# Kernel tuning notes

Hardware: AMD Instinct MI355X
Metric: run time of the kernel (lower is better)

The kernel has to match this reference:

```python
import jax, jax.numpy as jnp
import numpy as np

D_MODEL = 768
STATE_N = 16
BATCH = 8
SEQ = 2048


def setup_inputs() -> dict:
    key = jax.random.key(0)
    ks = jax.random.split(key, 12)
    d, n = D_MODEL, STATE_N
    s = 0.02
    inp = {
        "x": jax.random.normal(ks[0], (BATCH, SEQ, d), dtype=jnp.float32),
        # A_log init as in module: log(arange(1..N)) repeated over d_model
        "A_log": jnp.log(jnp.tile(jnp.arange(1, n + 1, dtype=jnp.float32)[None, :], (d, 1))),
        "D_param": jnp.ones((d,), dtype=jnp.float32),
        "B_proj_w": jax.random.normal(ks[1], (n, d), dtype=jnp.float32) * s,
        "C_proj_w": jax.random.normal(ks[2], (n, d), dtype=jnp.float32) * s,
        "delta_w": jax.random.normal(ks[3], (d, d), dtype=jnp.float32) * s,
        "delta_b": jax.random.normal(ks[4], (d,), dtype=jnp.float32) * s,
        "in_w": jax.random.normal(ks[5], (2 * d, d), dtype=jnp.float32) * s,
        "in_b": jax.random.normal(ks[6], (2 * d,), dtype=jnp.float32) * s,
        "out_w": jax.random.normal(ks[7], (d, d), dtype=jnp.float32) * s,
        "out_b": jax.random.normal(ks[8], (d,), dtype=jnp.float32) * s,
        "conv_w": jax.random.normal(ks[9], (d, 1, 3), dtype=jnp.float32) * s,  # depthwise [D,1,K]
        "conv_b": jax.random.normal(ks[10], (d,), dtype=jnp.float32) * s,
    }
    return inp


def _forward(x, A_log, D_param, B_proj_w, C_proj_w, delta_w, delta_b,
             in_w, in_b, out_w, out_b, conv_w, conv_b):
    A = -jnp.exp(A_log)  # [D, N]
    xz = jnp.einsum("bld,ed->ble", x, in_w) + in_b  # [B, L, 2D]
    x_in, z = jnp.split(xz, 2, axis=-1)
    # depthwise conv1d, padding=1, groups=D (cross-correlation, same as torch)
    x_c = jax.lax.conv_general_dilated(
        jnp.transpose(x_in, (0, 2, 1)), conv_w,
        window_strides=(1,), padding=((1, 1),),
        feature_group_count=x.shape[-1],
        dimension_numbers=("NCH", "OIH", "NCH"))
    x_conv = jnp.transpose(x_c, (0, 2, 1)) + conv_b  # [B, L, D]
    x_conv = jax.nn.silu(x_conv)
    delta = jax.nn.softplus(jnp.einsum("bld,ed->ble", x_conv, delta_w) + delta_b)  # [B,L,D]
    B_sel = jnp.einsum("bld,nd->bln", x_conv, B_proj_w)  # [B, L, N]
    C_sel = jnp.einsum("bld,nd->bln", x_conv, C_proj_w)  # [B, L, N]

    Bsz, L, D = x.shape
    N = A.shape[1]

    def step(h, t_in):
        dt, b_t, c_t, x_t = t_in  # [B,D], [B,N], [B,N], [B,D]
        A_bar = jnp.exp(dt[:, :, None] * A[None, :, :])           # [B,D,N]
        h = A_bar * h + (dt[:, :, None] * b_t[:, None, :]) * x_t[:, :, None]
        y_t = jnp.sum(h * c_t[:, None, :], axis=-1)               # [B,D]
        return h, y_t

    xs = (jnp.transpose(delta, (1, 0, 2)), jnp.transpose(B_sel, (1, 0, 2)),
          jnp.transpose(C_sel, (1, 0, 2)), jnp.transpose(x_conv, (1, 0, 2)))
    h0 = jnp.zeros((Bsz, D, N), dtype=x.dtype)
    _, ys = jax.lax.scan(step, h0, xs)
    y = jnp.transpose(ys, (1, 0, 2))  # [B, L, D]

    y = y + x_conv * D_param[None, None, :]
    y = y * jax.nn.silu(z)
    return jnp.einsum("bld,ed->ble", y, out_w) + out_b


def reference(x, A_log, D_param, B_proj_w, C_proj_w, delta_w, delta_b,
              in_w, in_b, out_w, out_b, conv_w, conv_b):
    return _forward(x, A_log, D_param, B_proj_w, C_proj_w, delta_w, delta_b,
                    in_w, in_b, out_w, out_b, conv_w, conv_b)
```

## Files before the change

### kernel.cpp

```cpp
#include <hip/hip_runtime.h>
#include <hip/hip_bf16.h>

#define D_MODEL 768
#define SEQL    2048
#define BATCH   8
#define NSTATE  16
#define NCHUNK  32
#define TCHUNK  64

typedef __attribute__((ext_vector_type(8))) short short8;
typedef __attribute__((ext_vector_type(4))) float f32x4;

typedef const __attribute__((address_space(1))) unsigned int gas1_t;
typedef __attribute__((address_space(3))) unsigned int las3_t;

__device__ __forceinline__ void gload_lds16(const void* g, void* l) {
  __builtin_amdgcn_global_load_lds((gas1_t*)g, (las3_t*)l, 16, 0, 0);
}

__global__ __launch_bounds__(256) void prep_all(
    const float* __restrict__ x, const float* __restrict__ in_w,
    const float* __restrict__ delta_w, const float* __restrict__ Bp,
    const float* __restrict__ Cp, const float* __restrict__ out_w,
    const float* __restrict__ A_log,
    __hip_bfloat16* __restrict__ xb, __hip_bfloat16* __restrict__ w_in,
    __hip_bfloat16* __restrict__ w_dbc, __hip_bfloat16* __restrict__ w_out,
    float* __restrict__ A2) {
  int i = blockIdx.x * 256 + threadIdx.x;
  if (i < 3145728) {
    int j = i * 4;
    float4 v = *(const float4*)(x + j);
    xb[j + 0] = __float2bfloat16(v.x);
    xb[j + 1] = __float2bfloat16(v.y);
    xb[j + 2] = __float2bfloat16(v.z);
    xb[j + 3] = __float2bfloat16(v.w);
    return;
  }
  i -= 3145728;
  if (i < 1536 * 768) { w_in[i] = __float2bfloat16(in_w[i]); return; }
  i -= 1536 * 768;
  if (i < 1024 * 768) {
    int row = i / 768, col = i - row * 768;
    float v;
    if (row < 768)      v = delta_w[row * 768 + col];
    else if (row < 784) v = Bp[(row - 768) * 768 + col];
    else if (row < 800) v = Cp[(row - 784) * 768 + col];
    else                v = 0.f;
    w_dbc[i] = __float2bfloat16(v);
    return;
  }
  i -= 1024 * 768;
  if (i < 768 * 768) { w_out[i] = __float2bfloat16(out_w[i]); return; }
  i -= 768 * 768;
  A2[i] = -expf(A_log[i]) * 1.44269504088896f;
}

template <int MODE>
__global__ __launch_bounds__(512, 2) void gemm256(
    const __hip_bfloat16* __restrict__ Amat, const __hip_bfloat16* __restrict__ Bw,
    const float* __restrict__ bias, void* __restrict__ out0,
    void* __restrict__ out1, void* __restrict__ out2, const int gxn) {
  constexpr int K = 768;
  __shared__ char lds[131072];
  const int tid  = threadIdx.x;
  const int lane = tid & 63, wave = tid >> 6;
  const int wr = wave >> 2, wc = wave & 3;

  const int nwg = gridDim.x, id = blockIdx.x;
  const int swz = (id & 7) * (nwg >> 3) + (id >> 3);
  const int tm = swz / gxn, tn = swz - tm * gxn;
  const int rowA0 = tm * 256, rowB0 = tn * 256;

  const int srow0 = tid >> 3;
  const int scol  = (((tid & 7) ^ (srow0 & 7)) << 3);
  const __hip_bfloat16* gA = Amat + (size_t)(rowA0 + srow0) * K + scol;
  const __hip_bfloat16* gB = Bw   + (size_t)(rowB0 + srow0) * K + scol;
  const int ldst = tid << 4;

  const int frow = lane & 15, fq = lane >> 4;
  const int fswz = (frow & 7) << 4;
  const int pc0 = (fq << 4) ^ fswz;
  const int pc1 = (64 | (fq << 4)) ^ fswz;
  const int aro = (wr * 64 + frow) << 7;
  const int bro = (wc * 32 + frow) << 7;

  f32x4 acc[2][2][4][2];
#pragma unroll
  for (int mh = 0; mh < 2; ++mh)
#pragma unroll
    for (int nh = 0; nh < 2; ++nh)
#pragma unroll
      for (int m = 0; m < 4; ++m)
#pragma unroll
        for (int n = 0; n < 2; ++n) acc[mh][nh][m][n] = (f32x4){0.f, 0.f, 0.f, 0.f};

#define STAGE_AH(d, h, kt)                                                      \
  {                                                                             \
    const __hip_bfloat16* s0 = gA + (size_t)((h)*128) * K + (kt)*64;            \
    char* d0 = lds + ((d) << 16) + ((h) << 14) + ldst;                          \
    gload_lds16(s0, d0);                                                        \
    gload_lds16(s0 + (size_t)64 * K, d0 + 8192);                                \
  }
#define STAGE_BH(d, h, kt)                                                      \
  {                                                                             \
    const __hip_bfloat16* s0 = gB + (size_t)((h)*128) * K + (kt)*64;            \
    char* d0 = lds + ((d) << 16) + 32768 + ((h) << 14) + ldst;                  \
    gload_lds16(s0, d0);                                                        \
    gload_lds16(s0 + (size_t)64 * K, d0 + 8192);                                \
  }

  short8 a[4][2], b[2][2];
#define LOADA(d, mh)                                                            \
  {                                                                             \
    const char* base = lds + ((d) << 16) + ((mh) << 14) + aro;                  \
    _Pragma("unroll") for (int m = 0; m < 4; ++m) {                             \
      const char* p = base + ((m * 16) << 7);                                   \
      a[m][0] = *(const short8*)(p + pc0);                                      \
      a[m][1] = *(const short8*)(p + pc1);                                      \
    }                                                                           \
  }
#define LOADB(d, nh)                                                            \
  {                                                                             \
    const char* base = lds + ((d) << 16) + 32768 + ((nh) << 14) + bro;          \
    _Pragma("unroll") for (int n = 0; n < 2; ++n) {                             \
      const char* p = base + ((n * 16) << 7);                                   \
      b[n][0] = *(const short8*)(p + pc0);                                      \
      b[n][1] = *(const short8*)(p + pc1);                                      \
    }                                                                           \
  }
#define MMA(mh, nh)                                                             \
  {                                                                             \
    __builtin_amdgcn_s_setprio(1);                                              \
    _Pragma("unroll") for (int m = 0; m < 4; ++m)                               \
    _Pragma("unroll") for (int n = 0; n < 2; ++n)                               \
    _Pragma("unroll") for (int ks = 0; ks < 2; ++ks)                            \
        acc[mh][nh][m][n] = __builtin_amdgcn_mfma_f32_16x16x32_bf16(            \
            a[m][ks], b[n][ks], acc[mh][nh][m][n], 0, 0, 0);                    \
    __builtin_amdgcn_s_setprio(0);                                              \
  }
#define VMW(n) asm volatile("s_waitcnt vmcnt(" #n ")" ::: "memory")

  STAGE_AH(0, 0, 0);
  STAGE_BH(0, 0, 0);
  STAGE_BH(0, 1, 0);
  STAGE_AH(0, 1, 0);

  constexpr int NT = K / 64;
  for (int kt = 0; kt < NT - 1; ++kt) {
    const int cur = kt & 1, nxt = cur ^ 1;
    VMW(4);
    __builtin_amdgcn_s_barrier();
    LOADA(cur, 0);
    LOADB(cur, 0);
    STAGE_AH(nxt, 0, kt + 1);
    MMA(0, 0);
    VMW(4);
    __builtin_amdgcn_s_barrier();
    LOADB(cur, 1);
    STAGE_BH(nxt, 0, kt + 1);
    MMA(0, 1);
    VMW(4);
    __builtin_amdgcn_s_barrier();
    LOADA(cur, 1);
    STAGE_BH(nxt, 1, kt + 1);
    MMA(1, 1);
    __builtin_amdgcn_s_barrier();
    LOADB(cur, 0);
    STAGE_AH(nxt, 1, kt + 1);
    MMA(1, 0);
  }
  {
    const int cur = (NT - 1) & 1;
    VMW(4);
    __builtin_amdgcn_s_barrier();
    LOADA(cur, 0);
    LOADB(cur, 0);
    MMA(0, 0);
    VMW(2);
    __builtin_amdgcn_s_barrier();
    LOADB(cur, 1);
    MMA(0, 1);
    VMW(0);
    __builtin_amdgcn_s_barrier();
    LOADA(cur, 1);
    MMA(1, 1);
    __builtin_amdgcn_s_barrier();
    LOADB(cur, 0);
    MMA(1, 0);
  }

#pragma unroll
  for (int mh = 0; mh < 2; ++mh)
#pragma unroll
    for (int nh = 0; nh < 2; ++nh)
#pragma unroll
      for (int m = 0; m < 4; ++m) {
        const int grow0 = rowA0 + mh * 128 + wr * 64 + m * 16 + fq * 4;
#pragma unroll
        for (int n = 0; n < 2; ++n) {
          const int gcol = rowB0 + nh * 128 + wc * 32 + n * 16 + frow;
#pragma unroll
          for (int i = 0; i < 4; ++i) {
            const size_t grow = grow0 + i;
            float v = acc[mh][nh][m][n][i];
            if (MODE == 0) {
              v += bias[gcol];
              if (gcol < 768)
                ((__hip_bfloat16*)out0)[grow * 768 + gcol] = __float2bfloat16(v);
              else
                ((__hip_bfloat16*)out1)[grow * 768 + gcol - 768] = __float2bfloat16(v);
            } else if (MODE == 1) {
              if (gcol < 768) {
                v += bias[gcol];
                float sp = (v > 20.f) ? v : log1pf(expf(v));
                ((__hip_bfloat16*)out0)[grow * 768 + gcol] = __float2bfloat16(sp);
              } else if (gcol < 784) {
                ((float*)out1)[grow * 16 + (gcol - 768)] = v;
              } else if (gcol < 800) {
                ((float*)out2)[grow * 16 + (gcol - 784)] = v;
              }
            } else {
              ((float*)out0)[grow * 768 + gcol] = v + bias[gcol];
            }
          }
        }
      }
#undef STAGE_AH
#undef STAGE_BH
#undef LOADA
#undef LOADB
#undef MMA
#undef VMW
}

__global__ __launch_bounds__(256) void conv_silu(
    const __hip_bfloat16* __restrict__ xin, const float* __restrict__ conv_w,
    const float* __restrict__ conv_b, __hip_bfloat16* __restrict__ xc) {
  const int idx = blockIdx.x * 256 + threadIdx.x;
  const int d = idx % 768;
  const int t = (idx / 768) % SEQL;
  const float w0 = conv_w[d * 3], w1 = conv_w[d * 3 + 1], w2 = conv_w[d * 3 + 2];
  float acc = conv_b[d];
  float xm = (t > 0)        ? __bfloat162float(xin[idx - 768]) : 0.f;
  float x0 = __bfloat162float(xin[idx]);
  float xp = (t < SEQL - 1) ? __bfloat162float(xin[idx + 768]) : 0.f;
  acc += w0 * xm + w1 * x0 + w2 * xp;
  const float sig = 1.f / (1.f + __expf(-acc));
  xc[idx] = __float2bfloat16(acc * sig);
}

__global__ __launch_bounds__(256) void scan_pass1(
    const __hip_bfloat16* __restrict__ delta, const __hip_bfloat16* __restrict__ xconv,
    const float* __restrict__ Bsel, const float* __restrict__ A2,
    float* __restrict__ sumdt, float* __restrict__ Sbuf) {
  const int d = blockIdx.x * 256 + threadIdx.x;
  const int b = blockIdx.y, c = blockIdx.z;
  __shared__ float sB[TCHUNK * 16];
  ((float4*)sB)[threadIdx.x] =
      ((const float4*)(Bsel + ((size_t)b * SEQL + c * TCHUNK) * 16))[threadIdx.x];
  __syncthreads();

  float a2[16];
#pragma unroll
  for (int n = 0; n < 16; ++n) a2[n] = A2[d * 16 + n];
  float h[16] = {};
  float sdt = 0.f;
  const size_t base = ((size_t)b * SEQL + c * TCHUNK) * 768 + d;
  for (int t = 0; t < TCHUNK; ++t) {
    const float dt = __bfloat162float(delta[base + (size_t)t * 768]);
    const float x = __bfloat162float(xconv[base + (size_t)t * 768]);
    sdt += dt;
    const float dtx = dt * x;
    const float* Br = &sB[t * 16];
#pragma unroll
    for (int n = 0; n < 16; ++n) {
      const float a = exp2f(dt * a2[n]);
      h[n] = fmaf(a, h[n], dtx * Br[n]);
    }
  }
  sumdt[((size_t)b * NCHUNK + c) * 768 + d] = sdt;
#pragma unroll
  for (int n = 0; n < 16; ++n)
    Sbuf[(((size_t)b * NCHUNK + c) * 16 + n) * 768 + d] = h[n];
}

__global__ __launch_bounds__(256) void scan_carry(
    const float* __restrict__ sumdt, const float* __restrict__ Sbuf,
    const float* __restrict__ A2, float* __restrict__ Hin) {
  const int idx = blockIdx.x * 256 + threadIdx.x;
  const int d = idx % 768;
  const int n = (idx / 768) & 15;
  const int b = idx / (768 * 16);
  const float a2 = A2[d * 16 + n];
  float h = 0.f;
  for (int c = 0; c < NCHUNK; ++c) {
    const size_t hb = (((size_t)(b * NCHUNK + c)) * 16 + n) * 768 + d;
    Hin[hb] = h;
    const float sd = sumdt[(b * NCHUNK + c) * 768 + d];
    h = fmaf(exp2f(sd * a2), h, Sbuf[hb]);
  }
}

__global__ __launch_bounds__(256) void scan_pass3(
    const __hip_bfloat16* __restrict__ delta, const __hip_bfloat16* __restrict__ xconv,
    const __hip_bfloat16* __restrict__ zb, const float* __restrict__ Bsel,
    const float* __restrict__ Csel, const float* __restrict__ A2,
    const float* __restrict__ Hin, const float* __restrict__ Dp,
    __hip_bfloat16* __restrict__ yg) {
  const int d = blockIdx.x * 256 + threadIdx.x;
  const int b = blockIdx.y, c = blockIdx.z;
  __shared__ float sB[TCHUNK * 16], sC[TCHUNK * 16];
  {
    const size_t off = ((size_t)b * SEQL + c * TCHUNK) * 16;
    ((float4*)sB)[threadIdx.x] = ((const float4*)(Bsel + off))[threadIdx.x];
    ((float4*)sC)[threadIdx.x] = ((const float4*)(Csel + off))[threadIdx.x];
  }
  __syncthreads();

  float a2[16];
#pragma unroll
  for (int n = 0; n < 16; ++n) a2[n] = A2[d * 16 + n];
  float h[16];
  {
    const size_t hb = ((size_t)b * NCHUNK + c) * 16 * 768 + d;
#pragma unroll
    for (int n = 0; n < 16; ++n) h[n] = Hin[hb + (size_t)n * 768];
  }
  const float Dpd = Dp[d];
  const size_t base = ((size_t)b * SEQL + c * TCHUNK) * 768 + d;
  for (int t = 0; t < TCHUNK; ++t) {
    const float dt = __bfloat162float(delta[base + (size_t)t * 768]);
    const float x = __bfloat162float(xconv[base + (size_t)t * 768]);
    const float dtx = dt * x;
    const float* Br = &sB[t * 16];
    const float* Cr = &sC[t * 16];
    float y = 0.f;
#pragma unroll
    for (int n = 0; n < 16; ++n) {
      const float a = exp2f(dt * a2[n]);
      h[n] = fmaf(a, h[n], dtx * Br[n]);
      y = fmaf(h[n], Cr[n], y);
    }
    const float z = __bfloat162float(zb[base + (size_t)t * 768]);
    const float sig = 1.f / (1.f + __expf(-z));
    const float out = (y + x * Dpd) * (z * sig);
    yg[base + (size_t)t * 768] = __float2bfloat16(out);
  }
}

extern "C" void kernel_launch(void* const* d_in, const int* in_sizes, int n_in,
                              void* d_out, int out_size, void* d_ws, size_t ws_size,
                              hipStream_t stream) {
  const float* x       = (const float*)d_in[0];
  const float* A_log   = (const float*)d_in[1];
  const float* D_param = (const float*)d_in[2];
  const float* B_proj  = (const float*)d_in[3];
  const float* C_proj  = (const float*)d_in[4];
  const float* delta_w = (const float*)d_in[5];
  const float* delta_b = (const float*)d_in[6];
  const float* in_w    = (const float*)d_in[7];
  const float* in_b    = (const float*)d_in[8];
  const float* out_w   = (const float*)d_in[9];
  const float* out_b   = (const float*)d_in[10];
  const float* conv_w  = (const float*)d_in[11];
  const float* conv_b  = (const float*)d_in[12];

  char* ws = (char*)d_ws;
  __hip_bfloat16* xb       = (__hip_bfloat16*)(ws + 0);
  __hip_bfloat16* w_in_b   = (__hip_bfloat16*)(ws + 25165824);
  __hip_bfloat16* w_dbc_b  = (__hip_bfloat16*)(ws + 27525120);
  __hip_bfloat16* w_out_b  = (__hip_bfloat16*)(ws + 29097984);
  float*          A2       = (float*)(ws + 30277632);
  __hip_bfloat16* xin_b    = (__hip_bfloat16*)(ws + 30326784);
  __hip_bfloat16* z_b      = (__hip_bfloat16*)(ws + 55492608);
  __hip_bfloat16* xconv_b  = (__hip_bfloat16*)(ws + 80658432);
  __hip_bfloat16* delta_bf = (__hip_bfloat16*)(ws + 105824256);
  float*          Bsel     = (float*)(ws + 130990080);
  float*          Csel     = (float*)(ws + 132038656);
  float*          sumdt    = (float*)(ws + 133087232);
  float*          Sbuf     = (float*)(ws + 133873664);
  float*          Hin      = (float*)(ws + 146456576);
  __hip_bfloat16* yg       = xb;

  const int BLD = BATCH * SEQL * D_MODEL;

  prep_all<<<22320, 256, 0, stream>>>(x, in_w, delta_w, B_proj, C_proj, out_w, A_log,
                                      xb, w_in_b, w_dbc_b, w_out_b, A2);
  gemm256<0><<<384, 512, 0, stream>>>(xb, w_in_b, in_b, xin_b, z_b, nullptr, 6);
  conv_silu<<<BLD / 256, 256, 0, stream>>>(xin_b, conv_w, conv_b, xconv_b);
  gemm256<1><<<256, 512, 0, stream>>>(xconv_b, w_dbc_b, delta_b, delta_bf, Bsel, Csel, 4);
  scan_pass1<<<dim3(3, BATCH, NCHUNK), 256, 0, stream>>>(delta_bf, xconv_b, Bsel, A2, sumdt, Sbuf);
  scan_carry<<<384, 256, 0, stream>>>(sumdt, Sbuf, A2, Hin);
  scan_pass3<<<dim3(3, BATCH, NCHUNK), 256, 0, stream>>>(delta_bf, xconv_b, z_b, Bsel, Csel, A2,
                                                         Hin, D_param, yg);
  gemm256<2><<<192, 512, 0, stream>>>(yg, w_out_b, out_b, (float*)d_out, nullptr, nullptr, 3);
}
```

Measured before the change: 363.8 us.

## Restructure GEMM LDS read/MMA schedule and vectorize depthwise conv by eight

The GEMM main loop now keeps separate register fragments for even/odd A halves and both B halves, so MMAs reuse fragments instead of re-reading LDS. It adds explicit barriers and lgkmcnt waits around the reads, and changes launch bounds to one workgroup per SIMD pair. The conv+SiLU kernel now processes eight channels per thread with 16-byte loads and stores, and bf16 conversions in the scan kernels use bit shifts. The aim is fewer LDS reads and better memory efficiency in conv, at the cost of more registers and extra barriers in the GEMM.

```diff
diff --git a/kernel.cpp b/kernel.cpp
--- a/kernel.cpp
+++ b/kernel.cpp
@@ -16,6 +16,14 @@
 
 __device__ __forceinline__ void gload_lds16(const void* g, void* l) {
   __builtin_amdgcn_global_load_lds((gas1_t*)g, (las3_t*)l, 16, 0, 0);
+}
+
+__device__ __forceinline__ float b2f(short s) {
+  return __uint_as_float(((unsigned)(unsigned short)s) << 16);
+}
+__device__ __forceinline__ short f2b(float f) {
+  __hip_bfloat16 h = __float2bfloat16(f);
+  return *reinterpret_cast<short*>(&h);
 }
 
 __global__ __launch_bounds__(256) void prep_all(
@@ -56,11 +64,12 @@
 }
 
 template <int MODE>
-__global__ __launch_bounds__(512, 2) void gemm256(
+__global__ __launch_bounds__(512, 1) void gemm256(
     const __hip_bfloat16* __restrict__ Amat, const __hip_bfloat16* __restrict__ Bw,
     const float* __restrict__ bias, void* __restrict__ out0,
     void* __restrict__ out1, void* __restrict__ out2, const int gxn) {
   constexpr int K = 768;
+  constexpr int NT = K / 64;
   __shared__ char lds[131072];
   const int tid  = threadIdx.x;
   const int lane = tid & 63, wave = tid >> 6;
@@ -109,84 +118,90 @@
     gload_lds16(s0 + (size_t)64 * K, d0 + 8192);                                \
   }
 
-  short8 a[4][2], b[2][2];
-#define LOADA(d, mh)                                                            \
+  short8 aE[4][2], aO[4][2], b0[2][2], b1[2][2];
+#define RD_A(dst, d, h)                                                         \
   {                                                                             \
-    const char* base = lds + ((d) << 16) + ((mh) << 14) + aro;                  \
+    const char* base = lds + ((d) << 16) + ((h) << 14) + aro;                   \
     _Pragma("unroll") for (int m = 0; m < 4; ++m) {                             \
       const char* p = base + ((m * 16) << 7);                                   \
-      a[m][0] = *(const short8*)(p + pc0);                                      \
-      a[m][1] = *(const short8*)(p + pc1);                                      \
+      dst[m][0] = *(const short8*)(p + pc0);                                    \
+      dst[m][1] = *(const short8*)(p + pc1);                                    \
     }                                                                           \
   }
-#define LOADB(d, nh)                                                            \
+#define RD_B(dst, d, h)                                                         \
   {                                                                             \
-    const char* base = lds + ((d) << 16) + 32768 + ((nh) << 14) + bro;          \
+    const char* base = lds + ((d) << 16) + 32768 + ((h) << 14) + bro;           \
     _Pragma("unroll") for (int n = 0; n < 2; ++n) {                             \
       const char* p = base + ((n * 16) << 7);                                   \
-      b[n][0] = *(const short8*)(p + pc0);                                      \
-      b[n][1] = *(const short8*)(p + pc1);                                      \
+      dst[n][0] = *(const short8*)(p + pc0);                                    \
+      dst[n][1] = *(const short8*)(p + pc1);                                    \
     }                                                                           \
   }
-#define MMA(mh, nh)                                                             \
+#define MMA(mh, nh, A, B)                                                       \
   {                                                                             \
     __builtin_amdgcn_s_setprio(1);                                              \
     _Pragma("unroll") for (int m = 0; m < 4; ++m)                               \
     _Pragma("unroll") for (int n = 0; n < 2; ++n)                               \
     _Pragma("unroll") for (int ks = 0; ks < 2; ++ks)                            \
         acc[mh][nh][m][n] = __builtin_amdgcn_mfma_f32_16x16x32_bf16(            \
-            a[m][ks], b[n][ks], acc[mh][nh][m][n], 0, 0, 0);                    \
+            A[m][ks], B[n][ks], acc[mh][nh][m][n], 0, 0, 0);                    \
     __builtin_amdgcn_s_setprio(0);                                              \
   }
 #define VMW(n) asm volatile("s_waitcnt vmcnt(" #n ")" ::: "memory")
+#define LGKM0  asm volatile("s_waitcnt lgkmcnt(0)" ::: "memory")
+#define BAR    __builtin_amdgcn_s_barrier()
 
   STAGE_AH(0, 0, 0);
   STAGE_BH(0, 0, 0);
   STAGE_BH(0, 1, 0);
   STAGE_AH(0, 1, 0);
-
-  constexpr int NT = K / 64;
+  VMW(4);
+  BAR;
+
   for (int kt = 0; kt < NT - 1; ++kt) {
     const int cur = kt & 1, nxt = cur ^ 1;
+    RD_A(aE, cur, 0);
+    RD_B(b0, cur, 0);
+    STAGE_AH(nxt, 0, kt + 1);
+    BAR; LGKM0;
+    MMA(0, 0, aE, b0);
     VMW(4);
-    __builtin_amdgcn_s_barrier();
-    LOADA(cur, 0);
-    LOADB(cur, 0);
-    STAGE_AH(nxt, 0, kt + 1);
-    MMA(0, 0);
+    BAR;
+    RD_B(b1, cur, 1);
+    STAGE_BH(nxt, 0, kt + 1);
+    BAR; LGKM0;
+    MMA(0, 1, aE, b1);
     VMW(4);
-    __builtin_amdgcn_s_barrier();
-    LOADB(cur, 1);
-    STAGE_BH(nxt, 0, kt + 1);
-    MMA(0, 1);
+    BAR;
+    RD_A(aO, cur, 1);
+    STAGE_BH(nxt, 1, kt + 1);
+    BAR; LGKM0;
+    MMA(1, 1, aO, b1);
+    BAR;
+    STAGE_AH(nxt, 1, kt + 1);
+    BAR;
+    MMA(1, 0, aO, b0);
     VMW(4);
-    __builtin_amdgcn_s_barrier();
-    LOADA(cur, 1);
-    STAGE_BH(nxt, 1, kt + 1);
-    MMA(1, 1);
-    __builtin_amdgcn_s_barrier();
-    LOADB(cur, 0);
-    STAGE_AH(nxt, 1, kt + 1);
-    MMA(1, 0);
+    BAR;
   }
   {
     const int cur = (NT - 1) & 1;
-    VMW(4);
-    __builtin_amdgcn_s_barrier();
-    LOADA(cur, 0);
-    LOADB(cur, 0);
-    MMA(0, 0);
+    RD_A(aE, cur, 0);
+    RD_B(b0, cur, 0);
+    BAR; LGKM0;
+    MMA(0, 0, aE, b0);
     VMW(2);
-    __builtin_amdgcn_s_barrier();
-    LOADB(cur, 1);
-    MMA(0, 1);
+    BAR;
+    RD_B(b1, cur, 1);
+    BAR; LGKM0;
+    MMA(0, 1, aE, b1);
     VMW(0);
-    __builtin_amdgcn_s_barrier();
-    LOADA(cur, 1);
-    MMA(1, 1);
-    __builtin_amdgcn_s_barrier();
-    LOADB(cur, 0);
-    MMA(1, 0);
+    BAR;
+    RD_A(aO, cur, 1);
+    BAR; LGKM0;
+    MMA(1, 1, aO, b1);
+    BAR;
+    MMA(1, 0, aO, b0);
   }
 
 #pragma unroll
@@ -227,26 +242,48 @@
       }
 #undef STAGE_AH
 #undef STAGE_BH
-#undef LOADA
-#undef LOADB
+#undef RD_A
+#undef RD_B
 #undef MMA
 #undef VMW
-}
-
-__global__ __launch_bounds__(256) void conv_silu(
+#undef LGKM0
+#undef BAR
+}
+
+__global__ __launch_bounds__(256) void conv_silu8(
     const __hip_bfloat16* __restrict__ xin, const float* __restrict__ conv_w,
     const float* __restrict__ conv_b, __hip_bfloat16* __restrict__ xc) {
   const int idx = blockIdx.x * 256 + threadIdx.x;
-  const int d = idx % 768;
-  const int t = (idx / 768) % SEQL;
-  const float w0 = conv_w[d * 3], w1 = conv_w[d * 3 + 1], w2 = conv_w[d * 3 + 2];
-  float acc = conv_b[d];
-  float xm = (t > 0)        ? __bfloat162float(xin[idx - 768]) : 0.f;
-  float x0 = __bfloat162float(xin[idx]);
-  float xp = (t < SEQL - 1) ? __bfloat162float(xin[idx + 768]) : 0.f;
-  acc += w0 * xm + w1 * x0 + w2 * xp;
-  const float sig = 1.f / (1.f + __expf(-acc));
-  xc[idx] = __float2bfloat16(acc * sig);
+  const int d8 = (idx % 96) * 8;
+  const int t  = (idx / 96) % SEQL;
+  const size_t base = (size_t)idx * 8;
+
+  short8 x0 = *(const short8*)(xin + base);
+  short8 xm = {}, xp = {};
+  if (t > 0)        xm = *(const short8*)(xin + base - 768);
+  if (t < SEQL - 1) xp = *(const short8*)(xin + base + 768);
+
+  const float4* cw4 = (const float4*)(conv_w + d8 * 3);
+  float4 cw[6];
+#pragma unroll
+  for (int q = 0; q < 6; ++q) cw[q] = cw4[q];
+  float4 cb0 = *(const float4*)(conv_b + d8);
+  float4 cb1 = *(const float4*)(conv_b + d8 + 4);
+  const float* cwf = (const float*)cw;
+  const float* cbf0 = (const float*)&cb0;
+  const float* cbf1 = (const float*)&cb1;
+
+  short8 r;
+#pragma unroll
+  for (int e = 0; e < 8; ++e) {
+    float acc = (e < 4) ? cbf0[e] : cbf1[e - 4];
+    acc = fmaf(cwf[e * 3 + 0], b2f(xm[e]), acc);
+    acc = fmaf(cwf[e * 3 + 1], b2f(x0[e]), acc);
+    acc = fmaf(cwf[e * 3 + 2], b2f(xp[e]), acc);
+    const float sig = 1.f / (1.f + __expf(-acc));
+    r[e] = f2b(acc * sig);
+  }
+  *(short8*)(xc + base) = r;
 }
 
 __global__ __launch_bounds__(256) void scan_pass1(
@@ -267,8 +304,8 @@
   float sdt = 0.f;
   const size_t base = ((size_t)b * SEQL + c * TCHUNK) * 768 + d;
   for (int t = 0; t < TCHUNK; ++t) {
-    const float dt = __bfloat162float(delta[base + (size_t)t * 768]);
-    const float x = __bfloat162float(xconv[base + (size_t)t * 768]);
+    const float dt = b2f(((const short*)delta)[base + (size_t)t * 768]);
+    const float x = b2f(((const short*)xconv)[base + (size_t)t * 768]);
     sdt += dt;
     const float dtx = dt * x;
     const float* Br = &sB[t * 16];
@@ -329,8 +366,8 @@
   const float Dpd = Dp[d];
   const size_t base = ((size_t)b * SEQL + c * TCHUNK) * 768 + d;
   for (int t = 0; t < TCHUNK; ++t) {
-    const float dt = __bfloat162float(delta[base + (size_t)t * 768]);
-    const float x = __bfloat162float(xconv[base + (size_t)t * 768]);
+    const float dt = b2f(((const short*)delta)[base + (size_t)t * 768]);
+    const float x = b2f(((const short*)xconv)[base + (size_t)t * 768]);
     const float dtx = dt * x;
     const float* Br = &sB[t * 16];
     const float* Cr = &sC[t * 16];
@@ -341,7 +378,7 @@
       h[n] = fmaf(a, h[n], dtx * Br[n]);
       y = fmaf(h[n], Cr[n], y);
     }
-    const float z = __bfloat162float(zb[base + (size_t)t * 768]);
+    const float z = b2f(((const short*)zb)[base + (size_t)t * 768]);
     const float sig = 1.f / (1.f + __expf(-z));
     const float out = (y + x * Dpd) * (z * sig);
     yg[base + (size_t)t * 768] = __float2bfloat16(out);
@@ -387,7 +424,7 @@
   prep_all<<<22320, 256, 0, stream>>>(x, in_w, delta_w, B_proj, C_proj, out_w, A_log,
                                       xb, w_in_b, w_dbc_b, w_out_b, A2);
   gemm256<0><<<384, 512, 0, stream>>>(xb, w_in_b, in_b, xin_b, z_b, nullptr, 6);
-  conv_silu<<<BLD / 256, 256, 0, stream>>>(xin_b, conv_w, conv_b, xconv_b);
+  conv_silu8<<<BLD / 8 / 256, 256, 0, stream>>>(xin_b, conv_w, conv_b, xconv_b);
   gemm256<1><<<256, 512, 0, stream>>>(xconv_b, w_dbc_b, delta_b, delta_bf, Bsel, Csel, 4);
   scan_pass1<<<dim3(3, BATCH, NCHUNK), 256, 0, stream>>>(delta_bf, xconv_b, Bsel, A2, sumdt, Sbuf);
   scan_carry<<<384, 256, 0, stream>>>(sumdt, Sbuf, A2, Hin);
```

New measurement: 351.3 us. -3.4%, faster.
